# Kernel optimization log

Measured on AMD Instinct MI355X. Metric: run time of the kernel, lower is better.

Reference implementation:

```python
import jax, jax.numpy as jnp
import numpy as np


def setup_inputs() -> dict:
    key = jax.random.key(0)
    k1, k2 = jax.random.split(key)
    inputs = jax.random.normal(k1, (64, 16, 64, 512), dtype=jnp.float32)
    cluster_centers = jax.random.normal(k2, (64, 512), dtype=jnp.float32) * 0.05
    return {"inputs": inputs, "cluster_centers": cluster_centers}


def reference(inputs, cluster_centers):
    # inputs: (B, H, W, C); cluster_centers: (K, C)
    B, H, W, C = inputs.shape
    K = cluster_centers.shape[0]
    x = inputs.reshape(B, H * W, C)                      # (B, N, C)
    # soft assignments: softmax over K of x @ centers^T
    logits = jnp.einsum('bnc,kc->bnk', x, cluster_centers)
    a = jax.nn.softmax(logits, axis=-1)                  # (B, N, K)
    # VLAD rewritten to avoid (B,N,K,C) residual tensor:
    # sum_n a[b,n,k] * (x[b,n,:] - c[k,:])
    #   = (a^T @ x)[b,k,:] - (sum_n a[b,n,k]) * c[k,:]
    agg = jnp.einsum('bnk,bnc->bkc', a, x)               # (B, K, C)
    a_sum = jnp.sum(a, axis=1)                           # (B, K)
    vlad = agg - a_sum[:, :, None] * cluster_centers[None, :, :]
    vlad = vlad.reshape(B, K * C)
    # tf.nn.l2_normalize: x / sqrt(max(sum(x^2), eps)), eps=1e-12
    norm = jnp.sqrt(jnp.maximum(jnp.sum(vlad * vlad, axis=-1, keepdims=True), 1e-12))
    return vlad / norm
```

## Files before the change

### kernel.cpp

```cpp
#include <hip/hip_runtime.h>
#include <stdint.h>

#define NB 64
#define NN 1024
#define CDIM 512
#define KK 64
#define XRS 38

typedef __attribute__((ext_vector_type(4))) float f32x4;
typedef __attribute__((ext_vector_type(8))) short short8;

__device__ __forceinline__ unsigned short f2bf(float f) {
  unsigned int u = __float_as_uint(f);
  return (unsigned short)((u + 0x7fffu + ((u >> 16) & 1u)) >> 16);
}

__device__ __forceinline__ void lgkm_barrier() {
  asm volatile("s_waitcnt lgkmcnt(0)" ::: "memory");
  __builtin_amdgcn_sched_barrier(0);
  __builtin_amdgcn_s_barrier();
}

__global__ __launch_bounds__(256) void k0_cvt(const float* __restrict__ cc,
                                              unsigned short* __restrict__ ccb) {
  int i = blockIdx.x * 256 + threadIdx.x;
  ccb[i] = f2bf(cc[i]);
}

__global__ __launch_bounds__(256) void k1_assign(const float* __restrict__ x,
    const unsigned short* __restrict__ ccb, unsigned short* __restrict__ a_t,
    unsigned int* __restrict__ xT32, float* __restrict__ a_sum) {
  const int b = blockIdx.y;
  const int n0 = blockIdx.x << 6;
  const int tid = threadIdx.x;
  const int w = tid >> 6;
  const int l = tid & 63;
  const int lr = l & 15;
  const int lg = l >> 4;

  __shared__ unsigned int xs[128 * XRS];
  __shared__ unsigned short a_sm[KK * 64];

  const float* xr = x + ((size_t)b * NN + n0 + (w << 4) + lr) * CDIM + (lg << 3);
  const unsigned short* cb = ccb + lr * CDIM + (lg << 3);
  const int n2 = (w << 3) + (lr >> 1);
  const int codd = l & 1;

  f32x4 acc0 = {0.f, 0.f, 0.f, 0.f}, acc1 = acc0, acc2 = acc0, acc3 = acc0;

  #pragma unroll 4
  for (int i = 0; i < 16; ++i) {
    const int cs = i << 5;
    f32x4 xa = *(const f32x4*)(xr + cs);
    f32x4 xb = *(const f32x4*)(xr + cs + 4);
    short8 af;
    af[0] = (short)f2bf(xa[0]); af[1] = (short)f2bf(xa[1]);
    af[2] = (short)f2bf(xa[2]); af[3] = (short)f2bf(xa[3]);
    af[4] = (short)f2bf(xb[0]); af[5] = (short)f2bf(xb[1]);
    af[6] = (short)f2bf(xb[2]); af[7] = (short)f2bf(xb[3]);
    short8 b0 = *(const short8*)(cb + cs);
    short8 b1 = *(const short8*)(cb + 16 * CDIM + cs);
    short8 b2 = *(const short8*)(cb + 32 * CDIM + cs);
    short8 b3 = *(const short8*)(cb + 48 * CDIM + cs);
    acc0 = __builtin_amdgcn_mfma_f32_16x16x32_bf16(af, b0, acc0, 0, 0, 0);
    acc1 = __builtin_amdgcn_mfma_f32_16x16x32_bf16(af, b1, acc1, 0, 0, 0);
    acc2 = __builtin_amdgcn_mfma_f32_16x16x32_bf16(af, b2, acc2, 0, 0, 0);
    acc3 = __builtin_amdgcn_mfma_f32_16x16x32_bf16(af, b3, acc3, 0, 0, 0);

    {
      const unsigned int* afu = (const unsigned int*)&af;
      const int cbase = ((i & 3) << 5) + (lg << 3) + codd;
      #pragma unroll
      for (int j = 0; j < 4; ++j) {
        unsigned int own = afu[j];
        unsigned int oth = (unsigned int)__shfl_xor((int)own, 1);
        unsigned int first  = codd ? oth : own;
        unsigned int second = codd ? own : oth;
        unsigned int lo = (first & 0xffffu) | (second << 16);
        unsigned int hi = (first >> 16) | (second & 0xffff0000u);
        xs[(cbase + (j << 1)) * XRS + n2] = codd ? hi : lo;
      }
    }
    if ((i & 3) == 3) {
      lgkm_barrier();
      const int s = i >> 2;
      const size_t gb = ((size_t)(b << 9) + (s << 7)) << 9;
      #pragma unroll
      for (int p = 0; p < 16; ++p) {
        const int f = (p << 8) + tid;
        unsigned int v = xs[(f >> 5) * XRS + (f & 31)];
        xT32[gb + (((size_t)(f >> 5)) << 9) + (n0 >> 1) + (f & 31)] = v;
      }
      lgkm_barrier();
    }
  }

  const int swzb = (lr & 7) << 3;
  float s0 = 0.f, s1 = 0.f, s2 = 0.f, s3 = 0.f;
  #pragma unroll
  for (int j = 0; j < 4; ++j) {
    float m = fmaxf(fmaxf(acc0[j], acc1[j]), fmaxf(acc2[j], acc3[j]));
    m = fmaxf(m, __shfl_xor(m, 1));
    m = fmaxf(m, __shfl_xor(m, 2));
    m = fmaxf(m, __shfl_xor(m, 4));
    m = fmaxf(m, __shfl_xor(m, 8));
    float e0 = __expf(acc0[j] - m);
    float e1 = __expf(acc1[j] - m);
    float e2 = __expf(acc2[j] - m);
    float e3 = __expf(acc3[j] - m);
    float s = e0 + e1 + e2 + e3;
    s += __shfl_xor(s, 1); s += __shfl_xor(s, 2);
    s += __shfl_xor(s, 4); s += __shfl_xor(s, 8);
    float inv = 1.0f / s;
    e0 *= inv; e1 *= inv; e2 *= inv; e3 *= inv;
    int r = (w << 4) + (lg << 2) + j;
    int rs = r ^ swzb;
    a_sm[( lr       << 6) + rs] = f2bf(e0);
    a_sm[((16 + lr) << 6) + rs] = f2bf(e1);
    a_sm[((32 + lr) << 6) + rs] = f2bf(e2);
    a_sm[((48 + lr) << 6) + rs] = f2bf(e3);
    s0 += e0; s1 += e1; s2 += e2; s3 += e3;
  }
  s0 += __shfl_xor(s0, 16); s0 += __shfl_xor(s0, 32);
  s1 += __shfl_xor(s1, 16); s1 += __shfl_xor(s1, 32);
  s2 += __shfl_xor(s2, 16); s2 += __shfl_xor(s2, 32);
  s3 += __shfl_xor(s3, 16); s3 += __shfl_xor(s3, 32);
  if (lg == 0) {
    atomicAdd(&a_sum[(b << 6) + lr],      s0);
    atomicAdd(&a_sum[(b << 6) + 16 + lr], s1);
    atomicAdd(&a_sum[(b << 6) + 32 + lr], s2);
    atomicAdd(&a_sum[(b << 6) + 48 + lr], s3);
  }
  __syncthreads();
  const unsigned int* au = (const unsigned int*)a_sm;
  for (int e = tid; e < 2048; e += 256) {
    int kc = e >> 5, nn2 = e & 31;
    unsigned int v = au[(kc << 5) + (nn2 ^ ((kc & 7) << 2))];
    *((unsigned int*)(a_t + (((size_t)((b << 6) + kc)) << 10) + n0) + nn2) = v;
  }
}

__global__ __launch_bounds__(256) void k2_agg(
    const unsigned short* __restrict__ a_t, const unsigned int* __restrict__ xT32,
    const float* __restrict__ cc, const float* __restrict__ a_sum,
    float* __restrict__ out, float* __restrict__ sumsq) {
  const int b = blockIdx.y;
  const int c0 = blockIdx.x << 6;
  const int tid = threadIdx.x;
  const int w = tid >> 6;
  const int l = tid & 63;
  const int lr = l & 15;
  const int lg = l >> 4;

  __shared__ unsigned int xs[2][64 * XRS];
  __shared__ float red[4];

  f32x4 acc[4];
  #pragma unroll
  for (int i = 0; i < 4; ++i) acc[i] = (f32x4){0.f, 0.f, 0.f, 0.f};

  const unsigned short* ap =
      a_t + (((size_t)((b << 6) + (w << 4) + lr)) << 10) + (lg << 3);
  const unsigned int* xg =
      xT32 + (((size_t)((b << 9) + c0 + (tid >> 5))) << 9) + (tid & 31);

  #pragma unroll
  for (int p = 0; p < 8; ++p) {
    const int f = (p << 8) + tid;
    xs[0][(f >> 5) * XRS + (f & 31)] = xg[(((size_t)p) << 12)];
  }
  short8 a_cur0 = *(const short8*)(ap);
  short8 a_cur1 = *(const short8*)(ap + 32);
  lgkm_barrier();

  for (int it = 0; it < 16; ++it) {
    const int cur = it & 1;
    unsigned int xr[8];
    short8 a_nxt0, a_nxt1;
    if (it < 15) {
      const int nu = (it + 1) << 5;
      #pragma unroll
      for (int p = 0; p < 8; ++p) xr[p] = xg[(((size_t)p) << 12) + nu];
      a_nxt0 = *(const short8*)(ap + ((it + 1) << 6));
      a_nxt1 = *(const short8*)(ap + ((it + 1) << 6) + 32);
    }
    #pragma unroll
    for (int ns = 0; ns < 64; ns += 32) {
      const short8 af = ns == 0 ? a_cur0 : a_cur1;
      #pragma unroll
      for (int ct = 0; ct < 4; ++ct) {
        const int row = (ct << 4) + lr;
        const unsigned long long* bp = (const unsigned long long*)
            &xs[cur][row * XRS + (ns >> 1) + (lg << 2)];
        union { unsigned long long q[2]; short8 s; } u;
        u.q[0] = bp[0];
        u.q[1] = bp[1];
        acc[ct] = __builtin_amdgcn_mfma_f32_16x16x32_bf16(af, u.s, acc[ct], 0, 0, 0);
      }
    }
    if (it < 15) {
      #pragma unroll
      for (int p = 0; p < 8; ++p) {
        const int f = (p << 8) + tid;
        xs[cur ^ 1][(f >> 5) * XRS + (f & 31)] = xr[p];
      }
      a_cur0 = a_nxt0;
      a_cur1 = a_nxt1;
    }
    lgkm_barrier();
  }

  float lsum = 0.f;
  #pragma unroll
  for (int ct = 0; ct < 4; ++ct) {
    #pragma unroll
    for (int j = 0; j < 4; ++j) {
      int k = (w << 4) + (lg << 2) + j;
      int c = c0 + (ct << 4) + lr;
      float v = acc[ct][j] - a_sum[(b << 6) + k] * cc[k * CDIM + c];
      out[((size_t)b << 15) + (k << 9) + c] = v;
      lsum += v * v;
    }
  }
  lsum += __shfl_xor(lsum, 1);  lsum += __shfl_xor(lsum, 2);
  lsum += __shfl_xor(lsum, 4);  lsum += __shfl_xor(lsum, 8);
  lsum += __shfl_xor(lsum, 16); lsum += __shfl_xor(lsum, 32);
  if (l == 0) red[w] = lsum;
  __syncthreads();
  if (tid == 0) atomicAdd(&sumsq[b], red[0] + red[1] + red[2] + red[3]);
}

__global__ __launch_bounds__(256) void k3_norm(float* __restrict__ out,
                                               const float* __restrict__ sumsq) {
  int idx = blockIdx.x * 256 + threadIdx.x;
  int b = idx >> 13;
  float s = sumsq[b];
  float scale = 1.0f / sqrtf(fmaxf(s, 1e-12f));
  f32x4* io = (f32x4*)out;
  f32x4 v = io[idx];
  v[0] *= scale; v[1] *= scale; v[2] *= scale; v[3] *= scale;
  io[idx] = v;
}

extern "C" void kernel_launch(void* const* d_in, const int* in_sizes, int n_in,
                              void* d_out, int out_size, void* d_ws, size_t ws_size,
                              hipStream_t stream) {
  const float* x  = (const float*)d_in[0];
  const float* cc = (const float*)d_in[1];
  float* out = (float*)d_out;
  char* ws = (char*)d_ws;
  unsigned short* a_t = (unsigned short*)ws;
  unsigned short* ccb = (unsigned short*)(ws + (8u << 20));
  float* a_sum = (float*)(ws + (8u << 20) + (64u << 10));
  float* sumsq = a_sum + NB * KK;
  unsigned int* xT32 = (unsigned int*)(ws + (16u << 20));

  (void)hipMemsetAsync(a_sum, 0, NB * KK * 4 + NB * 4, stream);
  k0_cvt<<<dim3((KK * CDIM) / 256), 256, 0, stream>>>(cc, ccb);
  k1_assign<<<dim3(16, NB), 256, 0, stream>>>(x, ccb, a_t, xT32, a_sum);
  k2_agg<<<dim3(8, NB), 256, 0, stream>>>(a_t, xT32, cc, a_sum, out, sumsq);
  k3_norm<<<dim3(2048), 256, 0, stream>>>(out, sumsq);
}
```

Baseline: 89.90 us.

## Give each wave a 64-row tile in assign kernel and recompute a_sum in agg

The assign kernel now gives each wave its own 64-row slab of n, with per-wave shared scratch for the x and assignment transposes. This removes block-wide barriers and reuses the cluster-center fragments across four row tiles. The grid shrinks to 4x64 blocks with launch_bounds(256,1). The a_sum atomics and their memset are dropped; k2 instead sums the bf16 assignment values it already loads and shuffles them to the lanes that need them. The risks are fewer blocks in k1 (256 in total), lower occupancy from the larger accumulator count, and a_sum now being built from bf16-rounded values.

```diff
diff --git a/kernel.cpp b/kernel.cpp
--- a/kernel.cpp
+++ b/kernel.cpp
@@ -5,7 +5,6 @@
 #define NN 1024
 #define CDIM 512
 #define KK 64
-#define XRS 38
 
 typedef __attribute__((ext_vector_type(4))) float f32x4;
 typedef __attribute__((ext_vector_type(8))) short short8;
@@ -13,6 +12,9 @@
 __device__ __forceinline__ unsigned short f2bf(float f) {
   unsigned int u = __float_as_uint(f);
   return (unsigned short)((u + 0x7fffu + ((u >> 16) & 1u)) >> 16);
+}
+__device__ __forceinline__ float bf2f(unsigned short h) {
+  return __uint_as_float(((unsigned int)h) << 16);
 }
 
 __device__ __forceinline__ void lgkm_barrier() {
@@ -27,123 +29,124 @@
   ccb[i] = f2bf(cc[i]);
 }
 
-__global__ __launch_bounds__(256) void k1_assign(const float* __restrict__ x,
-    const unsigned short* __restrict__ ccb, unsigned short* __restrict__ a_t,
-    unsigned int* __restrict__ xT32, float* __restrict__ a_sum) {
+__global__ __launch_bounds__(256, 1) void k1_assign(const float* __restrict__ x,
+    const unsigned short* __restrict__ ccb, unsigned int* __restrict__ a_t32,
+    unsigned int* __restrict__ xT32) {
   const int b = blockIdx.y;
-  const int n0 = blockIdx.x << 6;
   const int tid = threadIdx.x;
   const int w = tid >> 6;
   const int l = tid & 63;
   const int lr = l & 15;
   const int lg = l >> 4;
-
-  __shared__ unsigned int xs[128 * XRS];
-  __shared__ unsigned short a_sm[KK * 64];
-
-  const float* xr = x + ((size_t)b * NN + n0 + (w << 4) + lr) * CDIM + (lg << 3);
+  const int n0 = ((blockIdx.x << 2) + w) << 6;
+  const int codd = l & 1;
+
+  __shared__ unsigned int xsw_all[4][32 * 33];
+  __shared__ unsigned int asw_all[4][64 * 33];
+  unsigned int* xsw = xsw_all[w];
+  unsigned int* asw = asw_all[w];
+
+  const float* xr = x + ((size_t)b * NN + n0 + lr) * CDIM + (lg << 3);
   const unsigned short* cb = ccb + lr * CDIM + (lg << 3);
-  const int n2 = (w << 3) + (lr >> 1);
-  const int codd = l & 1;
-
-  f32x4 acc0 = {0.f, 0.f, 0.f, 0.f}, acc1 = acc0, acc2 = acc0, acc3 = acc0;
-
-  #pragma unroll 4
-  for (int i = 0; i < 16; ++i) {
-    const int cs = i << 5;
-    f32x4 xa = *(const f32x4*)(xr + cs);
-    f32x4 xb = *(const f32x4*)(xr + cs + 4);
-    short8 af;
-    af[0] = (short)f2bf(xa[0]); af[1] = (short)f2bf(xa[1]);
-    af[2] = (short)f2bf(xa[2]); af[3] = (short)f2bf(xa[3]);
-    af[4] = (short)f2bf(xb[0]); af[5] = (short)f2bf(xb[1]);
-    af[6] = (short)f2bf(xb[2]); af[7] = (short)f2bf(xb[3]);
-    short8 b0 = *(const short8*)(cb + cs);
-    short8 b1 = *(const short8*)(cb + 16 * CDIM + cs);
-    short8 b2 = *(const short8*)(cb + 32 * CDIM + cs);
-    short8 b3 = *(const short8*)(cb + 48 * CDIM + cs);
-    acc0 = __builtin_amdgcn_mfma_f32_16x16x32_bf16(af, b0, acc0, 0, 0, 0);
-    acc1 = __builtin_amdgcn_mfma_f32_16x16x32_bf16(af, b1, acc1, 0, 0, 0);
-    acc2 = __builtin_amdgcn_mfma_f32_16x16x32_bf16(af, b2, acc2, 0, 0, 0);
-    acc3 = __builtin_amdgcn_mfma_f32_16x16x32_bf16(af, b3, acc3, 0, 0, 0);
-
-    {
-      const unsigned int* afu = (const unsigned int*)&af;
-      const int cbase = ((i & 3) << 5) + (lg << 3) + codd;
-      #pragma unroll
-      for (int j = 0; j < 4; ++j) {
-        unsigned int own = afu[j];
+
+  f32x4 acc[4][4];
+  #pragma unroll
+  for (int i = 0; i < 4; ++i)
+    #pragma unroll
+    for (int j = 0; j < 4; ++j) acc[i][j] = (f32x4){0.f, 0.f, 0.f, 0.f};
+
+  #pragma unroll 2
+  for (int step = 0; step < 16; ++step) {
+    const int cs = step << 5;
+    short8 af[4];
+    #pragma unroll
+    for (int tn = 0; tn < 4; ++tn) {
+      f32x4 xa = *(const f32x4*)(xr + (size_t)(tn << 4) * CDIM + cs);
+      f32x4 xb = *(const f32x4*)(xr + (size_t)(tn << 4) * CDIM + cs + 4);
+      short8 t;
+      t[0] = (short)f2bf(xa[0]); t[1] = (short)f2bf(xa[1]);
+      t[2] = (short)f2bf(xa[2]); t[3] = (short)f2bf(xa[3]);
+      t[4] = (short)f2bf(xb[0]); t[5] = (short)f2bf(xb[1]);
+      t[6] = (short)f2bf(xb[2]); t[7] = (short)f2bf(xb[3]);
+      af[tn] = t;
+    }
+    short8 bq0 = *(const short8*)(cb + cs);
+    short8 bq1 = *(const short8*)(cb + 16 * CDIM + cs);
+    short8 bq2 = *(const short8*)(cb + 32 * CDIM + cs);
+    short8 bq3 = *(const short8*)(cb + 48 * CDIM + cs);
+    #pragma unroll
+    for (int tn = 0; tn < 4; ++tn) {
+      acc[tn][0] = __builtin_amdgcn_mfma_f32_16x16x32_bf16(af[tn], bq0, acc[tn][0], 0, 0, 0);
+      acc[tn][1] = __builtin_amdgcn_mfma_f32_16x16x32_bf16(af[tn], bq1, acc[tn][1], 0, 0, 0);
+      acc[tn][2] = __builtin_amdgcn_mfma_f32_16x16x32_bf16(af[tn], bq2, acc[tn][2], 0, 0, 0);
+      acc[tn][3] = __builtin_amdgcn_mfma_f32_16x16x32_bf16(af[tn], bq3, acc[tn][3], 0, 0, 0);
+    }
+    #pragma unroll
+    for (int tn = 0; tn < 4; ++tn) {
+      #pragma unroll
+      for (int q = 0; q < 4; ++q) {
+        unsigned int own = ((const unsigned int*)&af[tn])[q];
         unsigned int oth = (unsigned int)__shfl_xor((int)own, 1);
-        unsigned int first  = codd ? oth : own;
-        unsigned int second = codd ? own : oth;
-        unsigned int lo = (first & 0xffffu) | (second << 16);
-        unsigned int hi = (first >> 16) | (second & 0xffff0000u);
-        xs[(cbase + (j << 1)) * XRS + n2] = codd ? hi : lo;
-      }
-    }
-    if ((i & 3) == 3) {
-      lgkm_barrier();
-      const int s = i >> 2;
-      const size_t gb = ((size_t)(b << 9) + (s << 7)) << 9;
-      #pragma unroll
-      for (int p = 0; p < 16; ++p) {
-        const int f = (p << 8) + tid;
-        unsigned int v = xs[(f >> 5) * XRS + (f & 31)];
-        xT32[gb + (((size_t)(f >> 5)) << 9) + (n0 >> 1) + (f & 31)] = v;
-      }
-      lgkm_barrier();
-    }
-  }
-
-  const int swzb = (lr & 7) << 3;
-  float s0 = 0.f, s1 = 0.f, s2 = 0.f, s3 = 0.f;
-  #pragma unroll
-  for (int j = 0; j < 4; ++j) {
-    float m = fmaxf(fmaxf(acc0[j], acc1[j]), fmaxf(acc2[j], acc3[j]));
-    m = fmaxf(m, __shfl_xor(m, 1));
-    m = fmaxf(m, __shfl_xor(m, 2));
-    m = fmaxf(m, __shfl_xor(m, 4));
-    m = fmaxf(m, __shfl_xor(m, 8));
-    float e0 = __expf(acc0[j] - m);
-    float e1 = __expf(acc1[j] - m);
-    float e2 = __expf(acc2[j] - m);
-    float e3 = __expf(acc3[j] - m);
-    float s = e0 + e1 + e2 + e3;
-    s += __shfl_xor(s, 1); s += __shfl_xor(s, 2);
-    s += __shfl_xor(s, 4); s += __shfl_xor(s, 8);
-    float inv = 1.0f / s;
-    e0 *= inv; e1 *= inv; e2 *= inv; e3 *= inv;
-    int r = (w << 4) + (lg << 2) + j;
-    int rs = r ^ swzb;
-    a_sm[( lr       << 6) + rs] = f2bf(e0);
-    a_sm[((16 + lr) << 6) + rs] = f2bf(e1);
-    a_sm[((32 + lr) << 6) + rs] = f2bf(e2);
-    a_sm[((48 + lr) << 6) + rs] = f2bf(e3);
-    s0 += e0; s1 += e1; s2 += e2; s3 += e3;
-  }
-  s0 += __shfl_xor(s0, 16); s0 += __shfl_xor(s0, 32);
-  s1 += __shfl_xor(s1, 16); s1 += __shfl_xor(s1, 32);
-  s2 += __shfl_xor(s2, 16); s2 += __shfl_xor(s2, 32);
-  s3 += __shfl_xor(s3, 16); s3 += __shfl_xor(s3, 32);
-  if (lg == 0) {
-    atomicAdd(&a_sum[(b << 6) + lr],      s0);
-    atomicAdd(&a_sum[(b << 6) + 16 + lr], s1);
-    atomicAdd(&a_sum[(b << 6) + 32 + lr], s2);
-    atomicAdd(&a_sum[(b << 6) + 48 + lr], s3);
-  }
-  __syncthreads();
-  const unsigned int* au = (const unsigned int*)a_sm;
-  for (int e = tid; e < 2048; e += 256) {
-    int kc = e >> 5, nn2 = e & 31;
-    unsigned int v = au[(kc << 5) + (nn2 ^ ((kc & 7) << 2))];
-    *((unsigned int*)(a_t + (((size_t)((b << 6) + kc)) << 10) + n0) + nn2) = v;
-  }
-}
-
+        unsigned int v = codd ? ((oth >> 16) | (own & 0xffff0000u))
+                              : ((own & 0xffffu) | (oth << 16));
+        xsw[((lg << 3) + (q << 1) + codd) * 33 + (tn << 3) + (lr >> 1)] = v;
+      }
+    }
+    #pragma unroll
+    for (int i = 0; i < 16; ++i) {
+      const int row = (i << 1) + (l >> 5);
+      xT32[(((size_t)((b << 9) + cs + row)) << 9) + (n0 >> 1) + (l & 31)] =
+          xsw[row * 33 + (l & 31)];
+    }
+  }
+
+  #pragma unroll
+  for (int tn = 0; tn < 4; ++tn) {
+    #pragma unroll
+    for (int j = 0; j < 4; ++j) {
+      float m = fmaxf(fmaxf(acc[tn][0][j], acc[tn][1][j]),
+                      fmaxf(acc[tn][2][j], acc[tn][3][j]));
+      m = fmaxf(m, __shfl_xor(m, 1));
+      m = fmaxf(m, __shfl_xor(m, 2));
+      m = fmaxf(m, __shfl_xor(m, 4));
+      m = fmaxf(m, __shfl_xor(m, 8));
+      float e0 = __expf(acc[tn][0][j] - m);
+      float e1 = __expf(acc[tn][1][j] - m);
+      float e2 = __expf(acc[tn][2][j] - m);
+      float e3 = __expf(acc[tn][3][j] - m);
+      float s = e0 + e1 + e2 + e3;
+      s += __shfl_xor(s, 1); s += __shfl_xor(s, 2);
+      s += __shfl_xor(s, 4); s += __shfl_xor(s, 8);
+      float inv = 1.0f / s;
+      acc[tn][0][j] = e0 * inv;
+      acc[tn][1][j] = e1 * inv;
+      acc[tn][2][j] = e2 * inv;
+      acc[tn][3][j] = e3 * inv;
+    }
+  }
+  #pragma unroll
+  for (int tn = 0; tn < 4; ++tn)
+    #pragma unroll
+    for (int tk = 0; tk < 4; ++tk)
+      #pragma unroll
+      for (int jp = 0; jp < 2; ++jp) {
+        unsigned int v = (unsigned int)f2bf(acc[tn][tk][2 * jp]) |
+                         ((unsigned int)f2bf(acc[tn][tk][2 * jp + 1]) << 16);
+        asw[((tk << 4) + lr) * 33 + (tn << 3) + (lg << 1) + jp] = v;
+      }
+  #pragma unroll
+  for (int i = 0; i < 32; ++i) {
+    const int k = (i << 1) + (l >> 5);
+    a_t32[(((size_t)((b << 6) + k)) << 9) + (n0 >> 1) + (l & 31)] =
+        asw[k * 33 + (l & 31)];
+  }
+}
+
+#define XRS 38
 __global__ __launch_bounds__(256) void k2_agg(
     const unsigned short* __restrict__ a_t, const unsigned int* __restrict__ xT32,
-    const float* __restrict__ cc, const float* __restrict__ a_sum,
-    float* __restrict__ out, float* __restrict__ sumsq) {
+    const float* __restrict__ cc, float* __restrict__ out,
+    float* __restrict__ sumsq) {
   const int b = blockIdx.y;
   const int c0 = blockIdx.x << 6;
   const int tid = threadIdx.x;
@@ -158,6 +161,7 @@
   f32x4 acc[4];
   #pragma unroll
   for (int i = 0; i < 4; ++i) acc[i] = (f32x4){0.f, 0.f, 0.f, 0.f};
+  float ssum = 0.f;
 
   const unsigned short* ap =
       a_t + (((size_t)((b << 6) + (w << 4) + lr)) << 10) + (lg << 3);
@@ -184,6 +188,9 @@
       a_nxt0 = *(const short8*)(ap + ((it + 1) << 6));
       a_nxt1 = *(const short8*)(ap + ((it + 1) << 6) + 32);
     }
+    #pragma unroll
+    for (int i = 0; i < 8; ++i)
+      ssum += bf2f((unsigned short)a_cur0[i]) + bf2f((unsigned short)a_cur1[i]);
     #pragma unroll
     for (int ns = 0; ns < 64; ns += 32) {
       const short8 af = ns == 0 ? a_cur0 : a_cur1;
@@ -210,14 +217,18 @@
     lgkm_barrier();
   }
 
+  ssum += __shfl_xor(ssum, 16);
+  ssum += __shfl_xor(ssum, 32);
+
   float lsum = 0.f;
   #pragma unroll
-  for (int ct = 0; ct < 4; ++ct) {
-    #pragma unroll
-    for (int j = 0; j < 4; ++j) {
+  for (int j = 0; j < 4; ++j) {
+    const float asum_e = __shfl(ssum, (lg << 2) + j);
+    #pragma unroll
+    for (int ct = 0; ct < 4; ++ct) {
       int k = (w << 4) + (lg << 2) + j;
       int c = c0 + (ct << 4) + lr;
-      float v = acc[ct][j] - a_sum[(b << 6) + k] * cc[k * CDIM + c];
+      float v = acc[ct][j] - asum_e * cc[k * CDIM + c];
       out[((size_t)b << 15) + (k << 9) + c] = v;
       lsum += v * v;
     }
@@ -250,14 +261,14 @@
   float* out = (float*)d_out;
   char* ws = (char*)d_ws;
   unsigned short* a_t = (unsigned short*)ws;
+  unsigned int* a_t32 = (unsigned int*)ws;
   unsigned short* ccb = (unsigned short*)(ws + (8u << 20));
-  float* a_sum = (float*)(ws + (8u << 20) + (64u << 10));
-  float* sumsq = a_sum + NB * KK;
+  float* sumsq = (float*)(ws + (8u << 20) + (64u << 10));
   unsigned int* xT32 = (unsigned int*)(ws + (16u << 20));
 
-  (void)hipMemsetAsync(a_sum, 0, NB * KK * 4 + NB * 4, stream);
+  (void)hipMemsetAsync(sumsq, 0, NB * 4, stream);
   k0_cvt<<<dim3((KK * CDIM) / 256), 256, 0, stream>>>(cc, ccb);
-  k1_assign<<<dim3(16, NB), 256, 0, stream>>>(x, ccb, a_t, xT32, a_sum);
-  k2_agg<<<dim3(8, NB), 256, 0, stream>>>(a_t, xT32, cc, a_sum, out, sumsq);
+  k1_assign<<<dim3(4, NB), 256, 0, stream>>>(x, ccb, a_t32, xT32);
+  k2_agg<<<dim3(8, NB), 256, 0, stream>>>(a_t, xT32, cc, out, sumsq);
   k3_norm<<<dim3(2048), 256, 0, stream>>>(out, sumsq);
 }
```

Result: faster. 79.08 us (-12.0%).

## Stage x tile in LDS as bf16, transpose from LDS, compute a_sum in agg kernel

Applied to the files above, without the earlier changes.

k1_assign now loads the whole 64x512 x tile into LDS as bf16 with coalesced vector loads, then reads MFMA operands from LDS. The transposed xT32 copy is produced in one pass at the end of the kernel instead of through interleaved shuffle-and-barrier stages. The per-cluster assignment sums are no longer written with global atomics; k2_agg rebuilds them from the bf16 assignments it already loads, which also removes the a_sum memset. The cost is about 68KB of LDS per block, which limits occupancy, a serial load phase before any MFMA work, and a_sum computed from bf16-rounded values.

```diff
diff --git a/kernel.cpp b/kernel.cpp
--- a/kernel.cpp
+++ b/kernel.cpp
@@ -5,14 +5,18 @@
 #define NN 1024
 #define CDIM 512
 #define KK 64
-#define XRS 38
+#define XPAD 536
 
 typedef __attribute__((ext_vector_type(4))) float f32x4;
 typedef __attribute__((ext_vector_type(8))) short short8;
+typedef __attribute__((ext_vector_type(4))) unsigned short u16x4;
 
 __device__ __forceinline__ unsigned short f2bf(float f) {
   unsigned int u = __float_as_uint(f);
   return (unsigned short)((u + 0x7fffu + ((u >> 16) & 1u)) >> 16);
+}
+__device__ __forceinline__ float bf2f(unsigned short h) {
+  return __uint_as_float(((unsigned int)h) << 16);
 }
 
 __device__ __forceinline__ void lgkm_barrier() {
@@ -27,9 +31,9 @@
   ccb[i] = f2bf(cc[i]);
 }
 
-__global__ __launch_bounds__(256) void k1_assign(const float* __restrict__ x,
+__global__ __launch_bounds__(256, 2) void k1_assign(const float* __restrict__ x,
     const unsigned short* __restrict__ ccb, unsigned short* __restrict__ a_t,
-    unsigned int* __restrict__ xT32, float* __restrict__ a_sum) {
+    unsigned int* __restrict__ xT32) {
   const int b = blockIdx.y;
   const int n0 = blockIdx.x << 6;
   const int tid = threadIdx.x;
@@ -38,26 +42,30 @@
   const int lr = l & 15;
   const int lg = l >> 4;
 
-  __shared__ unsigned int xs[128 * XRS];
+  __shared__ unsigned short x_sm[64 * XPAD];
   __shared__ unsigned short a_sm[KK * 64];
 
-  const float* xr = x + ((size_t)b * NN + n0 + (w << 4) + lr) * CDIM + (lg << 3);
+  {
+    const float* xb = x + (((size_t)(b * NN + n0)) << 9);
+    #pragma unroll 4
+    for (int i = 0; i < 32; ++i) {
+      const int f4 = (i << 8) + tid;
+      const int n = f4 >> 7;
+      const int c4 = (f4 & 127) << 2;
+      f32x4 v = *(const f32x4*)(xb + ((size_t)n << 9) + c4);
+      u16x4 pk;
+      pk[0] = f2bf(v[0]); pk[1] = f2bf(v[1]);
+      pk[2] = f2bf(v[2]); pk[3] = f2bf(v[3]);
+      *(u16x4*)&x_sm[n * XPAD + c4] = pk;
+    }
+  }
+  __syncthreads();
+
   const unsigned short* cb = ccb + lr * CDIM + (lg << 3);
-  const int n2 = (w << 3) + (lr >> 1);
-  const int codd = l & 1;
-
   f32x4 acc0 = {0.f, 0.f, 0.f, 0.f}, acc1 = acc0, acc2 = acc0, acc3 = acc0;
-
   #pragma unroll 4
-  for (int i = 0; i < 16; ++i) {
-    const int cs = i << 5;
-    f32x4 xa = *(const f32x4*)(xr + cs);
-    f32x4 xb = *(const f32x4*)(xr + cs + 4);
-    short8 af;
-    af[0] = (short)f2bf(xa[0]); af[1] = (short)f2bf(xa[1]);
-    af[2] = (short)f2bf(xa[2]); af[3] = (short)f2bf(xa[3]);
-    af[4] = (short)f2bf(xb[0]); af[5] = (short)f2bf(xb[1]);
-    af[6] = (short)f2bf(xb[2]); af[7] = (short)f2bf(xb[3]);
+  for (int cs = 0; cs < CDIM; cs += 32) {
+    short8 af = *(const short8*)&x_sm[((w << 4) + lr) * XPAD + cs + (lg << 3)];
     short8 b0 = *(const short8*)(cb + cs);
     short8 b1 = *(const short8*)(cb + 16 * CDIM + cs);
     short8 b2 = *(const short8*)(cb + 32 * CDIM + cs);
@@ -66,37 +74,9 @@
     acc1 = __builtin_amdgcn_mfma_f32_16x16x32_bf16(af, b1, acc1, 0, 0, 0);
     acc2 = __builtin_amdgcn_mfma_f32_16x16x32_bf16(af, b2, acc2, 0, 0, 0);
     acc3 = __builtin_amdgcn_mfma_f32_16x16x32_bf16(af, b3, acc3, 0, 0, 0);
-
-    {
-      const unsigned int* afu = (const unsigned int*)&af;
-      const int cbase = ((i & 3) << 5) + (lg << 3) + codd;
-      #pragma unroll
-      for (int j = 0; j < 4; ++j) {
-        unsigned int own = afu[j];
-        unsigned int oth = (unsigned int)__shfl_xor((int)own, 1);
-        unsigned int first  = codd ? oth : own;
-        unsigned int second = codd ? own : oth;
-        unsigned int lo = (first & 0xffffu) | (second << 16);
-        unsigned int hi = (first >> 16) | (second & 0xffff0000u);
-        xs[(cbase + (j << 1)) * XRS + n2] = codd ? hi : lo;
-      }
-    }
-    if ((i & 3) == 3) {
-      lgkm_barrier();
-      const int s = i >> 2;
-      const size_t gb = ((size_t)(b << 9) + (s << 7)) << 9;
-      #pragma unroll
-      for (int p = 0; p < 16; ++p) {
-        const int f = (p << 8) + tid;
-        unsigned int v = xs[(f >> 5) * XRS + (f & 31)];
-        xT32[gb + (((size_t)(f >> 5)) << 9) + (n0 >> 1) + (f & 31)] = v;
-      }
-      lgkm_barrier();
-    }
   }
 
   const int swzb = (lr & 7) << 3;
-  float s0 = 0.f, s1 = 0.f, s2 = 0.f, s3 = 0.f;
   #pragma unroll
   for (int j = 0; j < 4; ++j) {
     float m = fmaxf(fmaxf(acc0[j], acc1[j]), fmaxf(acc2[j], acc3[j]));
@@ -119,31 +99,42 @@
     a_sm[((16 + lr) << 6) + rs] = f2bf(e1);
     a_sm[((32 + lr) << 6) + rs] = f2bf(e2);
     a_sm[((48 + lr) << 6) + rs] = f2bf(e3);
-    s0 += e0; s1 += e1; s2 += e2; s3 += e3;
-  }
-  s0 += __shfl_xor(s0, 16); s0 += __shfl_xor(s0, 32);
-  s1 += __shfl_xor(s1, 16); s1 += __shfl_xor(s1, 32);
-  s2 += __shfl_xor(s2, 16); s2 += __shfl_xor(s2, 32);
-  s3 += __shfl_xor(s3, 16); s3 += __shfl_xor(s3, 32);
-  if (lg == 0) {
-    atomicAdd(&a_sum[(b << 6) + lr],      s0);
-    atomicAdd(&a_sum[(b << 6) + 16 + lr], s1);
-    atomicAdd(&a_sum[(b << 6) + 32 + lr], s2);
-    atomicAdd(&a_sum[(b << 6) + 48 + lr], s3);
   }
   __syncthreads();
-  const unsigned int* au = (const unsigned int*)a_sm;
-  for (int e = tid; e < 2048; e += 256) {
-    int kc = e >> 5, nn2 = e & 31;
-    unsigned int v = au[(kc << 5) + (nn2 ^ ((kc & 7) << 2))];
-    *((unsigned int*)(a_t + (((size_t)((b << 6) + kc)) << 10) + n0) + nn2) = v;
-  }
-}
-
+
+  {
+    const unsigned int* au = (const unsigned int*)a_sm;
+    #pragma unroll
+    for (int e0 = 0; e0 < 2048; e0 += 256) {
+      int e = e0 + tid;
+      int kc = e >> 5, n2 = e & 31;
+      unsigned int v = au[(kc << 5) + (n2 ^ ((kc & 7) << 2))];
+      *((unsigned int*)(a_t + (((size_t)((b << 6) + kc)) << 10) + n0) + n2) = v;
+    }
+  }
+
+  {
+    const int nq = tid & 31;
+    const int cp0 = tid >> 5;
+    const size_t gb = (((size_t)b) << 18) + (n0 >> 1) + nq;
+    #pragma unroll 4
+    for (int i = 0; i < 32; ++i) {
+      const int c0 = ((i << 3) + cp0) << 1;
+      unsigned int lo = *(const unsigned int*)&x_sm[(nq << 1) * XPAD + c0];
+      unsigned int hi = *(const unsigned int*)&x_sm[((nq << 1) + 1) * XPAD + c0];
+      unsigned int v0 = (lo & 0xffffu) | (hi << 16);
+      unsigned int v1 = (lo >> 16) | (hi & 0xffff0000u);
+      xT32[gb + (((size_t)c0) << 9)] = v0;
+      xT32[gb + (((size_t)(c0 + 1)) << 9)] = v1;
+    }
+  }
+}
+
+#define XRS 38
 __global__ __launch_bounds__(256) void k2_agg(
     const unsigned short* __restrict__ a_t, const unsigned int* __restrict__ xT32,
-    const float* __restrict__ cc, const float* __restrict__ a_sum,
-    float* __restrict__ out, float* __restrict__ sumsq) {
+    const float* __restrict__ cc, float* __restrict__ out,
+    float* __restrict__ sumsq) {
   const int b = blockIdx.y;
   const int c0 = blockIdx.x << 6;
   const int tid = threadIdx.x;
@@ -158,6 +149,7 @@
   f32x4 acc[4];
   #pragma unroll
   for (int i = 0; i < 4; ++i) acc[i] = (f32x4){0.f, 0.f, 0.f, 0.f};
+  float ssum = 0.f;
 
   const unsigned short* ap =
       a_t + (((size_t)((b << 6) + (w << 4) + lr)) << 10) + (lg << 3);
@@ -184,6 +176,9 @@
       a_nxt0 = *(const short8*)(ap + ((it + 1) << 6));
       a_nxt1 = *(const short8*)(ap + ((it + 1) << 6) + 32);
     }
+    #pragma unroll
+    for (int i = 0; i < 8; ++i)
+      ssum += bf2f((unsigned short)a_cur0[i]) + bf2f((unsigned short)a_cur1[i]);
     #pragma unroll
     for (int ns = 0; ns < 64; ns += 32) {
       const short8 af = ns == 0 ? a_cur0 : a_cur1;
@@ -210,14 +205,18 @@
     lgkm_barrier();
   }
 
+  ssum += __shfl_xor(ssum, 16);
+  ssum += __shfl_xor(ssum, 32);
+
   float lsum = 0.f;
   #pragma unroll
-  for (int ct = 0; ct < 4; ++ct) {
-    #pragma unroll
-    for (int j = 0; j < 4; ++j) {
+  for (int j = 0; j < 4; ++j) {
+    const float asum_e = __shfl(ssum, (lg << 2) + j);
+    #pragma unroll
+    for (int ct = 0; ct < 4; ++ct) {
       int k = (w << 4) + (lg << 2) + j;
       int c = c0 + (ct << 4) + lr;
-      float v = acc[ct][j] - a_sum[(b << 6) + k] * cc[k * CDIM + c];
+      float v = acc[ct][j] - asum_e * cc[k * CDIM + c];
       out[((size_t)b << 15) + (k << 9) + c] = v;
       lsum += v * v;
     }
@@ -251,13 +250,12 @@
   char* ws = (char*)d_ws;
   unsigned short* a_t = (unsigned short*)ws;
   unsigned short* ccb = (unsigned short*)(ws + (8u << 20));
-  float* a_sum = (float*)(ws + (8u << 20) + (64u << 10));
-  float* sumsq = a_sum + NB * KK;
+  float* sumsq = (float*)(ws + (8u << 20) + (64u << 10));
   unsigned int* xT32 = (unsigned int*)(ws + (16u << 20));
 
-  (void)hipMemsetAsync(a_sum, 0, NB * KK * 4 + NB * 4, stream);
+  (void)hipMemsetAsync(sumsq, 0, NB * 4, stream);
   k0_cvt<<<dim3((KK * CDIM) / 256), 256, 0, stream>>>(cc, ccb);
-  k1_assign<<<dim3(16, NB), 256, 0, stream>>>(x, ccb, a_t, xT32, a_sum);
-  k2_agg<<<dim3(8, NB), 256, 0, stream>>>(a_t, xT32, cc, a_sum, out, sumsq);
+  k1_assign<<<dim3(16, NB), 256, 0, stream>>>(x, ccb, a_t, xT32);
+  k2_agg<<<dim3(8, NB), 256, 0, stream>>>(a_t, xT32, cc, out, sumsq);
   k3_norm<<<dim3(2048), 256, 0, stream>>>(out, sumsq);
 }
```

Result: slower. 101.4 us (+12.8%).
